# Performance work log

Hardware: AMD Instinct MI355X
Metric: run time of the kernel (lower is better)

## Reference

```python
import jax, jax.numpy as jnp
import numpy as np

EPS = 1e-5
DN = ('NCHW', 'OIHW', 'NCHW')

def _conv(x, w):
    return jax.lax.conv_general_dilated(x, w, (1, 1), 'SAME', dimension_numbers=DN)

def _bn(x, g, b, m, v):
    scale = (g * jax.lax.rsqrt(v + EPS)).reshape(1, -1, 1, 1)
    shift = (b - m * g * jax.lax.rsqrt(v + EPS)).reshape(1, -1, 1, 1)
    return x * scale + shift

def _convbn(x, w, g, b, m, v):
    return jax.nn.relu(_bn(_conv(x, w), g, b, m, v))

def _top_pool(x):
    # CornerNet TopPool: out[..., i, :] = max over rows >= i (reverse cummax along H)
    return jax.lax.cummax(x, axis=2, reverse=True)

def _left_pool(x):
    # CornerNet LeftPool: out[..., :, j] = max over cols >= j (reverse cummax along W)
    return jax.lax.cummax(x, axis=3, reverse=True)

def _mk_convbn(key, cin, cout, k):
    ks = jax.random.split(key, 5)
    w = jax.random.normal(ks[0], (cout, cin, k, k), jnp.float32) * (1.0 / np.sqrt(cin * k * k))
    g = jax.random.uniform(ks[1], (cout,), jnp.float32, 0.5, 1.5)
    b = jax.random.normal(ks[2], (cout,), jnp.float32) * 0.1
    m = jax.random.normal(ks[3], (cout,), jnp.float32) * 0.1
    v = jax.random.uniform(ks[4], (cout,), jnp.float32, 0.5, 1.5)
    return w, g, b, m, v

def setup_inputs() -> dict:
    key = jax.random.key(0)
    ks = jax.random.split(key, 12)
    dim, mid, B, H, W = 256, 128, 8, 128, 128
    d = {}
    d['x'] = jax.random.normal(ks[0], (B, dim, H, W), jnp.float32)
    for name, kk in [('lc1', ks[1]), ('p1c1', ks[2]), ('lc2', ks[3]), ('p2c1', ks[4])]:
        w, g, b, m, v = _mk_convbn(kk, dim, mid, 3)
        d[name + '_w'], d[name + '_g'], d[name + '_b'], d[name + '_m'], d[name + '_v'] = w, g, b, m, v
    d['p1lc_w'] = jax.random.normal(ks[5], (mid, mid, 3, 3), jnp.float32) * (1.0 / np.sqrt(mid * 9))
    d['p2lc_w'] = jax.random.normal(ks[6], (mid, mid, 3, 3), jnp.float32) * (1.0 / np.sqrt(mid * 9))
    w, g, b, m, v = _mk_convbn(ks[7], mid, dim, 3)
    d['pconv1_w'], d['pbn1_g'], d['pbn1_b'], d['pbn1_m'], d['pbn1_v'] = w, g, b, m, v
    w, g, b, m, v = _mk_convbn(ks[8], dim, dim, 1)
    d['conv1_w'], d['bn1_g'], d['bn1_b'], d['bn1_m'], d['bn1_v'] = w, g, b, m, v
    w, g, b, m, v = _mk_convbn(ks[9], dim, dim, 3)
    d['c2_w'], d['c2_g'], d['c2_b'], d['c2_m'], d['c2_v'] = w, g, b, m, v
    return d

def reference(x, lc1_w, lc1_g, lc1_b, lc1_m, lc1_v, p1c1_w, p1c1_g, p1c1_b, p1c1_m, p1c1_v, lc2_w, lc2_g, lc2_b, lc2_m, lc2_v, p2c1_w, p2c1_g, p2c1_b, p2c1_m, p2c1_v, p1lc_w, p2lc_w, pconv1_w, pbn1_g, pbn1_b, pbn1_m, pbn1_v, conv1_w, bn1_g, bn1_b, bn1_m, bn1_v, c2_w, c2_g, c2_b, c2_m, c2_v):
    look_conv1 = _convbn(x, lc1_w, lc1_g, lc1_b, lc1_m, lc1_v)
    p1_conv1 = _convbn(x, p1c1_w, p1c1_g, p1c1_b, p1c1_m, p1c1_v)
    look2 = _left_pool(look_conv1)
    p1_look = _conv(p1_conv1 + look2, p1lc_w)
    pool1 = _top_pool(p1_look)
    look_conv2 = _convbn(x, lc2_w, lc2_g, lc2_b, lc2_m, lc2_v)
    p2_conv1 = _convbn(x, p2c1_w, p2c1_g, p2c1_b, p2c1_m, p2c1_v)
    look1 = _top_pool(look_conv2)
    p2_look = _conv(p2_conv1 + look1, p2lc_w)
    pool2 = _left_pool(p2_look)
    p_bn1 = _bn(_conv(pool1 + pool2, pconv1_w), pbn1_g, pbn1_b, pbn1_m, pbn1_v)
    bn1 = _bn(_conv(x, conv1_w), bn1_g, bn1_b, bn1_m, bn1_v)
    relu1 = jax.nn.relu(p_bn1 + bn1)
    return _convbn(relu1, c2_w, c2_g, c2_b, c2_m, c2_v)
```

## Files before the change

### kernel.cpp

```cpp
#include <hip/hip_runtime.h>
#include <hip/hip_bf16.h>
#include <stdint.h>
#include <math.h>

typedef __bf16 bf16;
typedef __bf16 bf16x8 __attribute__((ext_vector_type(8)));
typedef float f32x4 __attribute__((ext_vector_type(4)));


__global__ void k_x_split(const float* __restrict__ in, bf16* __restrict__ out) {
  __shared__ float t[32][33];
  const int b = blockIdx.z;
  const int p0 = blockIdx.x << 5, c0 = blockIdx.y << 5;
  const int tx = threadIdx.x, ty = threadIdx.y;
  const float* ib = in + (size_t)b * 256 * 16384;
  bf16* ob = out + (size_t)b * 16384 * 512;
#pragma unroll
  for (int k = 0; k < 32; k += 8)
    t[ty + k][tx] = ib[(size_t)(c0 + ty + k) * 16384 + p0 + tx];
  __syncthreads();
#pragma unroll
  for (int k = 0; k < 32; k += 8) {
    float v = t[tx][ty + k];
    bf16 hv = (bf16)v;
    bf16 lv = (bf16)(v - (float)hv);
    ob[(size_t)(p0 + ty + k) * 512 + c0 + tx] = hv;
    ob[(size_t)(p0 + ty + k) * 512 + 256 + c0 + tx] = lv;
  }
}

__global__ void k_repack2(const float* __restrict__ src, bf16* __restrict__ dst,
                          int Cout, int Cin, int taps, int coutTotal, int coff) {
  int tid = blockIdx.x * 256 + threadIdx.x;
  int total = Cout * Cin * taps;
  if (tid >= total) return;
  int t = tid % taps;
  int rest = tid / taps;
  int ci = rest % Cin;
  int co = rest / Cin;
  float w = src[tid];
  bf16 wh = (bf16)w;
  bf16 wl = (bf16)(w - (float)wh);
  int nchunk = Cin >> 5;
  size_t segsz = (size_t)coutTotal * Cin;
  size_t base = (((size_t)(2 * t) * nchunk + (ci >> 5)) * coutTotal + coff + co) * 32
                + (ci & 31);
  dst[base] = wh;
  dst[base + segsz] = wl;
}

__global__ void k_bncoef(const float* __restrict__ g, const float* __restrict__ b,
                         const float* __restrict__ m, const float* __restrict__ v,
                         float* __restrict__ sc, float* __restrict__ sh, int n) {
  int c = blockIdx.x * 256 + threadIdx.x;
  if (c >= n) return;
  float s = g[c] * (1.0f / sqrtf(v[c] + 1e-5f));
  sc[c] = s;
  sh[c] = b[c] - m[c] * s;
}

template <int NTAPS>
__global__ __launch_bounds__(256, 3)
void k_conv(const bf16* __restrict__ in, int Cin, int rowStride,
            const bf16* __restrict__ Wr, int Cout,
            const float* __restrict__ scale, const float* __restrict__ shift,
            const bf16* __restrict__ addbuf, int relu,
            int out_mode, void* __restrict__ out) {
  constexpr int R = (NTAPS == 9) ? 3 : 1;
  __shared__ bf16 b_slab[2 * R * 132 * 32];
  const int bx = blockIdx.x;
  const int bb = bx & 7, h = (bx >> 3) & 127;
  const int row = bb * 128 + h;
  const int co_block = blockIdx.y << 7;
  const int tid = threadIdx.x;
  const int lane = tid & 63, wave = tid >> 6;
  const int wm = (wave >> 1) << 6, wn = (wave & 1) << 6;
  const int quad = lane >> 4, l15 = lane & 15;
  const int nchunk = Cin >> 5;
  const size_t segsz = (size_t)Cout * Cin;

  f32x4 acc[4][4];
#pragma unroll
  for (int i = 0; i < 4; ++i)
#pragma unroll
    for (int j = 0; j < 4; ++j)
#pragma unroll
      for (int r = 0; r < 4; ++r) acc[i][j][r] = 0.0f;

  {
    uint4 z; z.x = z.y = z.z = z.w = 0u;
    for (int u = tid; u < 2 * R * 2 * 4; u += 256) {
      int g = u & 3, e = (u >> 2) & 1, plane = u >> 3;
      bf16* d = &b_slab[((size_t)plane * 132 + (e ? 129 : 0)) * 32 + g * 8];
      *(uint4*)d = z;
    }
    if (R == 3 && (h == 0 || h == 127)) {
      int rr = (h == 0) ? 0 : 2;
      for (int u = tid; u < 2 * 132 * 4; u += 256) {
        int g = u & 3, p = (u >> 2) % 132, hl = (u >> 2) / 132;
        bf16* d = &b_slab[((size_t)(hl * R + rr) * 132 + p) * 32 + g * 8];
        *(uint4*)d = z;
      }
    }
  }

  for (int cb = 0; cb < Cin; cb += 32) {
    for (int u = wave; u < 2 * R * 8; u += 4) {
      int plane = u >> 3, sub = u & 7;
      int hl, rr;
      if (R == 3) { hl = plane >= 3; rr = plane - (hl ? 3 : 0); }
      else        { hl = plane; rr = 0; }
      int hi = h + rr - (R == 3 ? 1 : 0);
      if ((unsigned)hi < 128u) {
        int p = 1 + sub * 16 + (lane >> 2);
        int gsw = (lane & 3) ^ ((p >> 1) & 3);
        const bf16* src = in + (size_t)((bb * 128 + hi) * 128 + (p - 1)) * rowStride
                          + (size_t)hl * Cin + cb + gsw * 8;
        bf16* dst = &b_slab[(size_t)(plane * 132 + 1 + sub * 16) * 32];
        __builtin_amdgcn_global_load_lds(
            (const __attribute__((address_space(1))) uint32_t*)src,
            (__attribute__((address_space(3))) uint32_t*)dst, 16, 0, 0);
      }
    }
    __syncthreads();
#pragma unroll
    for (int tap = 0; tap < NTAPS; ++tap) {
      const int rr = (R == 3) ? (tap / 3) : 0;
      const int wc = (R == 3) ? (tap % 3) : 1;
      const int bH = rr * 132;
      const int bL = (R + rr) * 132;
      const int p0 = wn + l15 + wc;
      const int sw8 = (((p0 >> 1) & 3) ^ quad) << 3;
      const bf16* Ah = Wr + (((size_t)(2 * tap) * nchunk + (cb >> 5)) * Cout
                             + co_block + wm + l15) * 32 + quad * 8;
      const bf16* Al = Ah + segsz;
      bf16x8 afH[4], afL[4], bfH[4], bfL[4];
#pragma unroll
      for (int i = 0; i < 4; ++i) {
        afH[i] = *(const bf16x8*)(Ah + (size_t)i * 16 * 32);
        afL[i] = *(const bf16x8*)(Al + (size_t)i * 16 * 32);
      }
#pragma unroll
      for (int j = 0; j < 4; ++j) {
        const int p_idx = p0 + j * 16;
        bfH[j] = *(const bf16x8*)&b_slab[(size_t)(bH + p_idx) * 32 + sw8];
        bfL[j] = *(const bf16x8*)&b_slab[(size_t)(bL + p_idx) * 32 + sw8];
      }
#pragma unroll
      for (int i = 0; i < 4; ++i)
#pragma unroll
        for (int j = 0; j < 4; ++j) {
          acc[i][j] = __builtin_amdgcn_mfma_f32_16x16x32_bf16(afH[i], bfH[j], acc[i][j], 0, 0, 0);
          acc[i][j] = __builtin_amdgcn_mfma_f32_16x16x32_bf16(afH[i], bfL[j], acc[i][j], 0, 0, 0);
          acc[i][j] = __builtin_amdgcn_mfma_f32_16x16x32_bf16(afL[i], bfH[j], acc[i][j], 0, 0, 0);
        }
    }
    __syncthreads();
  }

#pragma unroll
  for (int i = 0; i < 4; ++i) {
    const int co = co_block + wm + i * 16 + (quad << 2);
#pragma unroll
    for (int j = 0; j < 4; ++j) {
      const int pos = wn + j * 16 + l15;
      float v[4];
#pragma unroll
      for (int r = 0; r < 4; ++r) v[r] = acc[i][j][r];
      if (scale) {
#pragma unroll
        for (int r = 0; r < 4; ++r) v[r] = v[r] * scale[co + r] + shift[co + r];
      }
      if (addbuf) {
        const bf16* ah = addbuf + (size_t)(row * 128 + pos) * (2 * Cout) + co;
        const bf16* al = ah + Cout;
#pragma unroll
        for (int r = 0; r < 4; ++r) v[r] += (float)ah[r] + (float)al[r];
      }
      if (relu) {
#pragma unroll
        for (int r = 0; r < 4; ++r) v[r] = fmaxf(v[r], 0.0f);
      }
      if (out_mode == 0) {
        bf16* ob = (bf16*)out;
        union { bf16 hv[4]; uint2 u; } ph, pl;
#pragma unroll
        for (int r = 0; r < 4; ++r) {
          ph.hv[r] = (bf16)v[r];
          pl.hv[r] = (bf16)(v[r] - (float)ph.hv[r]);
        }
        const size_t base = (size_t)(row * 128 + pos) * (2 * Cout);
        *(uint2*)&ob[base + co] = ph.u;
        *(uint2*)&ob[base + Cout + co] = pl.u;
      } else if (out_mode == 1) {
        float* of = (float*)out;
        float4 pk = make_float4(v[0], v[1], v[2], v[3]);
        *(float4*)&of[(size_t)(row * 128 + pos) * Cout + co] = pk;
      } else {
        float* of = (float*)out;
#pragma unroll
        for (int r = 0; r < 4; ++r)
          of[((size_t)(bb * Cout + co + r) * 128 + h) * 128 + pos] = v[r];
      }
    }
  }
}

__global__ void k_pool_s1(bf16* __restrict__ y) {
  int tid = blockIdx.x * 256 + threadIdx.x;
  int c = tid & 127, h = (tid >> 7) & 127, b = tid >> 14;
  bf16* base = y + (size_t)((b * 128 + h) * 128) * 512;
  float run = -INFINITY;
  for (int w = 127; w >= 0; --w) {
    bf16* p = base + (size_t)w * 512;
    float look = (float)p[c] + (float)p[256 + c];
    float padd = (float)p[128 + c] + (float)p[384 + c];
    run = fmaxf(run, look);
    float sum = run + padd;
    bf16 hv = (bf16)sum;
    p[c] = hv;
    p[128 + c] = (bf16)(sum - (float)hv);
  }
}
__global__ void k_pool_s2(bf16* __restrict__ y) {
  int tid = blockIdx.x * 256 + threadIdx.x;
  int c = tid & 127, w = (tid >> 7) & 127, b = tid >> 14;
  bf16* base = y + ((size_t)b * 16384 + w) * 512;
  float run = -INFINITY;
  for (int hh = 127; hh >= 0; --hh) {
    bf16* p = base + (size_t)hh * 65536;
    float look = (float)p[c] + (float)p[256 + c];
    float padd = (float)p[128 + c] + (float)p[384 + c];
    run = fmaxf(run, look);
    float sum = run + padd;
    bf16 hv = (bf16)sum;
    p[c] = hv;
    p[128 + c] = (bf16)(sum - (float)hv);
  }
}
__global__ void k_tpool_f(float* __restrict__ buf) {
  int tid = blockIdx.x * 256 + threadIdx.x;
  int c = tid & 127, w = (tid >> 7) & 127, b = tid >> 14;
  float* p = buf + ((size_t)b * 16384 + w) * 128 + c;
  float run = -INFINITY;
  for (int hh = 127; hh >= 0; --hh) {
    run = fmaxf(run, p[(size_t)hh * 16384]);
    p[(size_t)hh * 16384] = run;
  }
}
__global__ void k_lpool_add_f(const float* __restrict__ in, const float* __restrict__ addb,
                              bf16* __restrict__ out) {
  int tid = blockIdx.x * 256 + threadIdx.x;
  int c = tid & 127, h = (tid >> 7) & 127, b = tid >> 14;
  const float* p = in + (size_t)((b * 128 + h) * 128) * 128 + c;
  const float* a = addb + (size_t)((b * 128 + h) * 128) * 128 + c;
  bf16* o = out + (size_t)((b * 128 + h) * 128) * 256;
  float run = -INFINITY;
  for (int w = 127; w >= 0; --w) {
    run = fmaxf(run, p[(size_t)w * 128]);
    float sum = run + a[(size_t)w * 128];
    bf16 hv = (bf16)sum;
    o[(size_t)w * 256 + c] = hv;
    o[(size_t)w * 256 + 128 + c] = (bf16)(sum - (float)hv);
  }
}

extern "C" void kernel_launch(void* const* d_in, const int* in_sizes, int n_in,
                              void* d_out, int out_size, void* d_ws, size_t ws_size,
                              hipStream_t stream) {
  (void)in_sizes; (void)n_in; (void)out_size; (void)ws_size;
#define INF(i) ((const float*)d_in[i])
  char* ws = (char*)d_ws;
  const size_t MB = 1 << 20;
  bf16* wrA  = (bf16*)(ws + 0);
  bf16* wrB  = (bf16*)(ws + 2359296);
  bf16* wrp1 = (bf16*)(ws + 4718592);
  bf16* wrp2 = (bf16*)(ws + 5308416);
  bf16* wrpc = (bf16*)(ws + 5898240);
  bf16* wrc1 = (bf16*)(ws + 7077888);
  bf16* wrc2 = (bf16*)(ws + 7340032);
  float* scA  = (float*)(ws + 9699328);
  float* shA  = (float*)(ws + 9703424);
  float* scB  = (float*)(ws + 9707520);
  float* shB  = (float*)(ws + 9711616);
  float* scp  = (float*)(ws + 9715712);
  float* shp  = (float*)(ws + 9719808);
  float* scb  = (float*)(ws + 9723904);
  float* shb  = (float*)(ws + 9728000);
  float* scc2 = (float*)(ws + 9732096);
  float* shc2 = (float*)(ws + 9736192);
  bf16*  x_hl  = (bf16*)(ws + 10 * MB);
  bf16*  bnrel = (bf16*)(ws + 138 * MB);
  float* p1lk  = (float*)(ws + 266 * MB);
  float* p2lk  = (float*)(ws + 10 * MB);
  bf16*  psum  = (bf16*)(ws + 74 * MB);
  bf16*  yscr  = (bf16*)d_out;

  k_x_split<<<dim3(512, 8, 8), dim3(32, 8), 0, stream>>>(INF(0), x_hl);

  k_repack2<<<1152, 256, 0, stream>>>(INF(1),  wrA,  128, 256, 9, 256, 0);
  k_repack2<<<1152, 256, 0, stream>>>(INF(6),  wrA,  128, 256, 9, 256, 128);
  k_repack2<<<1152, 256, 0, stream>>>(INF(11), wrB,  128, 256, 9, 256, 0);
  k_repack2<<<1152, 256, 0, stream>>>(INF(16), wrB,  128, 256, 9, 256, 128);
  k_repack2<<<576,  256, 0, stream>>>(INF(21), wrp1, 128, 128, 9, 128, 0);
  k_repack2<<<576,  256, 0, stream>>>(INF(22), wrp2, 128, 128, 9, 128, 0);
  k_repack2<<<1152, 256, 0, stream>>>(INF(23), wrpc, 256, 128, 9, 256, 0);
  k_repack2<<<256,  256, 0, stream>>>(INF(28), wrc1, 256, 256, 1, 256, 0);
  k_repack2<<<2304, 256, 0, stream>>>(INF(33), wrc2, 256, 256, 9, 256, 0);

  k_bncoef<<<1, 256, 0, stream>>>(INF(2),  INF(3),  INF(4),  INF(5),  scA,       shA,       128);
  k_bncoef<<<1, 256, 0, stream>>>(INF(7),  INF(8),  INF(9),  INF(10), scA + 128, shA + 128, 128);
  k_bncoef<<<1, 256, 0, stream>>>(INF(12), INF(13), INF(14), INF(15), scB,       shB,       128);
  k_bncoef<<<1, 256, 0, stream>>>(INF(17), INF(18), INF(19), INF(20), scB + 128, shB + 128, 128);
  k_bncoef<<<1, 256, 0, stream>>>(INF(24), INF(25), INF(26), INF(27), scp, shp, 256);
  k_bncoef<<<1, 256, 0, stream>>>(INF(29), INF(30), INF(31), INF(32), scb, shb, 256);
  k_bncoef<<<1, 256, 0, stream>>>(INF(34), INF(35), INF(36), INF(37), scc2, shc2, 256);

  k_conv<1><<<dim3(1024, 2), 256, 0, stream>>>(x_hl, 256, 512, wrc1, 256, scb, shb, nullptr, 0, 0, bnrel);
  k_conv<9><<<dim3(1024, 2), 256, 0, stream>>>(x_hl, 256, 512, wrA, 256, scA, shA, nullptr, 1, 0, yscr);
  k_pool_s1<<<512, 256, 0, stream>>>(yscr);
  k_conv<9><<<dim3(1024, 1), 256, 0, stream>>>(yscr, 128, 512, wrp1, 128, nullptr, nullptr, nullptr, 0, 1, p1lk);
  k_conv<9><<<dim3(1024, 2), 256, 0, stream>>>(x_hl, 256, 512, wrB, 256, scB, shB, nullptr, 1, 0, yscr);
  k_pool_s2<<<512, 256, 0, stream>>>(yscr);
  k_conv<9><<<dim3(1024, 1), 256, 0, stream>>>(yscr, 128, 512, wrp2, 128, nullptr, nullptr, nullptr, 0, 1, p2lk);
  k_tpool_f<<<512, 256, 0, stream>>>(p1lk);
  k_lpool_add_f<<<512, 256, 0, stream>>>(p2lk, p1lk, psum);
  k_conv<9><<<dim3(1024, 2), 256, 0, stream>>>(psum, 128, 256, wrpc, 256, scp, shp, bnrel, 1, 0, bnrel);
  k_conv<9><<<dim3(1024, 2), 256, 0, stream>>>(bnrel, 256, 512, wrc2, 256, scc2, shc2, nullptr, 1, 2, (float*)d_out);
#undef INF
}
```

Measured before the change: 2.291 ms.

## Split staging into hi/lo halves and overlap next-chunk loads with MFMA

Restructures the conv main loop so the hi and lo halves of the bf16-split input are staged separately. The next chunk's hi half loads while the current lo-half MFMAs run, and vice versa, with manual vmcnt waits and raw s_barrier in place of full __syncthreads. Out-of-range rows are redirected to a dummy LDS buffer so every wave issues the same number of loads, which keeps the vmcnt counting uniform. It also raises wave priority around the MFMA blocks. The aim is to hide global-to-LDS latency behind compute, at the cost of fragile wait counts and a redundant extra load on the last iteration.

```diff
diff --git a/kernel.cpp b/kernel.cpp
--- a/kernel.cpp
+++ b/kernel.cpp
@@ -68,6 +68,7 @@
             int out_mode, void* __restrict__ out) {
   constexpr int R = (NTAPS == 9) ? 3 : 1;
   __shared__ bf16 b_slab[2 * R * 132 * 32];
+  __shared__ bf16 dummy_lds[512];
   const int bx = blockIdx.x;
   const int bb = bx & 7, h = (bx >> 3) & 127;
   const int row = bb * 128 + h;
@@ -103,60 +104,105 @@
       }
     }
   }
+  __syncthreads();
+
+  auto stage_half = [&](int hl, int cb) {
+    for (int u = wave; u < R * 8; u += 4) {
+      int rr = u >> 3, sub = u & 7;
+      int plane = hl * R + rr;
+      int hi = h + rr - (R == 3 ? 1 : 0);
+      bool ok = (unsigned)hi < 128u;
+      int hic = ok ? hi : h;
+      int p = 1 + sub * 16 + (lane >> 2);
+      int gsw = (lane & 3) ^ ((p >> 1) & 3);
+      const bf16* src = in + (size_t)((bb * 128 + hic) * 128 + (p - 1)) * rowStride
+                        + (size_t)hl * Cin + cb + gsw * 8;
+      bf16* dst = ok ? &b_slab[(size_t)(plane * 132 + 1 + sub * 16) * 32]
+                     : dummy_lds;
+      __builtin_amdgcn_global_load_lds(
+          (const __attribute__((address_space(1))) uint32_t*)src,
+          (__attribute__((address_space(3))) uint32_t*)dst, 16, 0, 0);
+    }
+  };
+
+#define WAIT_VM()                                                        \
+  do {                                                                   \
+    __builtin_amdgcn_sched_barrier(0);                                   \
+    if constexpr (R == 3) asm volatile("s_waitcnt vmcnt(6)" ::: "memory"); \
+    else                  asm volatile("s_waitcnt vmcnt(2)" ::: "memory"); \
+    __builtin_amdgcn_sched_barrier(0);                                   \
+  } while (0)
+
+  stage_half(0, 0);
+  stage_half(1, 0);
 
   for (int cb = 0; cb < Cin; cb += 32) {
-    for (int u = wave; u < 2 * R * 8; u += 4) {
-      int plane = u >> 3, sub = u & 7;
-      int hl, rr;
-      if (R == 3) { hl = plane >= 3; rr = plane - (hl ? 3 : 0); }
-      else        { hl = plane; rr = 0; }
-      int hi = h + rr - (R == 3 ? 1 : 0);
-      if ((unsigned)hi < 128u) {
-        int p = 1 + sub * 16 + (lane >> 2);
-        int gsw = (lane & 3) ^ ((p >> 1) & 3);
-        const bf16* src = in + (size_t)((bb * 128 + hi) * 128 + (p - 1)) * rowStride
-                          + (size_t)hl * Cin + cb + gsw * 8;
-        bf16* dst = &b_slab[(size_t)(plane * 132 + 1 + sub * 16) * 32];
-        __builtin_amdgcn_global_load_lds(
-            (const __attribute__((address_space(1))) uint32_t*)src,
-            (__attribute__((address_space(3))) uint32_t*)dst, 16, 0, 0);
-      }
-    }
-    __syncthreads();
+    WAIT_VM();
+    __builtin_amdgcn_s_barrier();
 #pragma unroll
     for (int tap = 0; tap < NTAPS; ++tap) {
       const int rr = (R == 3) ? (tap / 3) : 0;
       const int wc = (R == 3) ? (tap % 3) : 1;
       const int bH = rr * 132;
+      const int p0 = wn + l15 + wc;
+      const int sw8 = (((p0 >> 1) & 3) ^ quad) << 3;
+      const bf16* Ah = Wr + (((size_t)(2 * tap) * nchunk + (cb >> 5)) * Cout
+                             + co_block + wm + l15) * 32 + quad * 8;
+      const bf16* Al = Ah + segsz;
+      bf16x8 afH[4], afL[4], bfH[4];
+#pragma unroll
+      for (int i = 0; i < 4; ++i) {
+        afH[i] = *(const bf16x8*)(Ah + (size_t)i * 16 * 32);
+        afL[i] = *(const bf16x8*)(Al + (size_t)i * 16 * 32);
+      }
+#pragma unroll
+      for (int j = 0; j < 4; ++j)
+        bfH[j] = *(const bf16x8*)&b_slab[(size_t)(bH + p0 + j * 16) * 32 + sw8];
+      __builtin_amdgcn_s_setprio(1);
+#pragma unroll
+      for (int i = 0; i < 4; ++i)
+#pragma unroll
+        for (int j = 0; j < 4; ++j) {
+          acc[i][j] = __builtin_amdgcn_mfma_f32_16x16x32_bf16(afH[i], bfH[j], acc[i][j], 0, 0, 0);
+          acc[i][j] = __builtin_amdgcn_mfma_f32_16x16x32_bf16(afL[i], bfH[j], acc[i][j], 0, 0, 0);
+        }
+      __builtin_amdgcn_s_setprio(0);
+    }
+    __builtin_amdgcn_s_barrier();
+    {
+      int nb = (cb + 32 < Cin) ? cb + 32 : cb;
+      stage_half(0, nb);
+    }
+    WAIT_VM();
+    __builtin_amdgcn_s_barrier();
+#pragma unroll
+    for (int tap = 0; tap < NTAPS; ++tap) {
+      const int rr = (R == 3) ? (tap / 3) : 0;
+      const int wc = (R == 3) ? (tap % 3) : 1;
       const int bL = (R + rr) * 132;
       const int p0 = wn + l15 + wc;
       const int sw8 = (((p0 >> 1) & 3) ^ quad) << 3;
       const bf16* Ah = Wr + (((size_t)(2 * tap) * nchunk + (cb >> 5)) * Cout
                              + co_block + wm + l15) * 32 + quad * 8;
-      const bf16* Al = Ah + segsz;
-      bf16x8 afH[4], afL[4], bfH[4], bfL[4];
-#pragma unroll
-      for (int i = 0; i < 4; ++i) {
+      bf16x8 afH[4], bfL[4];
+#pragma unroll
+      for (int i = 0; i < 4; ++i)
         afH[i] = *(const bf16x8*)(Ah + (size_t)i * 16 * 32);
-        afL[i] = *(const bf16x8*)(Al + (size_t)i * 16 * 32);
-      }
-#pragma unroll
-      for (int j = 0; j < 4; ++j) {
-        const int p_idx = p0 + j * 16;
-        bfH[j] = *(const bf16x8*)&b_slab[(size_t)(bH + p_idx) * 32 + sw8];
-        bfL[j] = *(const bf16x8*)&b_slab[(size_t)(bL + p_idx) * 32 + sw8];
-      }
+#pragma unroll
+      for (int j = 0; j < 4; ++j)
+        bfL[j] = *(const bf16x8*)&b_slab[(size_t)(bL + p0 + j * 16) * 32 + sw8];
+      __builtin_amdgcn_s_setprio(1);
 #pragma unroll
       for (int i = 0; i < 4; ++i)
 #pragma unroll
-        for (int j = 0; j < 4; ++j) {
-          acc[i][j] = __builtin_amdgcn_mfma_f32_16x16x32_bf16(afH[i], bfH[j], acc[i][j], 0, 0, 0);
+        for (int j = 0; j < 4; ++j)
           acc[i][j] = __builtin_amdgcn_mfma_f32_16x16x32_bf16(afH[i], bfL[j], acc[i][j], 0, 0, 0);
-          acc[i][j] = __builtin_amdgcn_mfma_f32_16x16x32_bf16(afL[i], bfH[j], acc[i][j], 0, 0, 0);
-        }
-    }
-    __syncthreads();
-  }
+      __builtin_amdgcn_s_setprio(0);
+    }
+    __builtin_amdgcn_s_barrier();
+    if (cb + 32 < Cin) stage_half(1, cb + 32);
+  }
+#undef WAIT_VM
 
 #pragma unroll
   for (int i = 0; i < 4; ++i) {
```

Result: slower. 2.598 ms (+13.4%).

## Split conv tiles to half-width rows and double-buffer LDS input staging

Applied to the files above, without the earlier changes.

The conv kernel now covers 64 output pixels per block instead of a full 128-pixel row, so twice as many blocks launch. Each wave owns 32 output channels across all 64 pixels. The input slab is double-buffered in LDS and the next channel chunk's global_load_lds is issued during the last tap's MFMAs, so loads overlap compute and one barrier per chunk is dropped. In exchange, the halo column is loaded separately and per-block tiles are smaller, which raises weight reloads and lowers MFMA reuse per B fragment.

```diff
diff --git a/kernel.cpp b/kernel.cpp
--- a/kernel.cpp
+++ b/kernel.cpp
@@ -67,21 +67,23 @@
             const bf16* __restrict__ addbuf, int relu,
             int out_mode, void* __restrict__ out) {
   constexpr int R = (NTAPS == 9) ? 3 : 1;
-  __shared__ bf16 b_slab[2 * R * 132 * 32];
+  constexpr int PL = 2 * R;
+  constexpr int BUF = PL * 66 * 32;
+  __shared__ bf16 b_slab[2 * BUF];
   const int bx = blockIdx.x;
   const int bb = bx & 7, h = (bx >> 3) & 127;
+  const int w0 = (bx >> 10) << 6;
   const int row = bb * 128 + h;
   const int co_block = blockIdx.y << 7;
   const int tid = threadIdx.x;
   const int lane = tid & 63, wave = tid >> 6;
-  const int wm = (wave >> 1) << 6, wn = (wave & 1) << 6;
   const int quad = lane >> 4, l15 = lane & 15;
   const int nchunk = Cin >> 5;
   const size_t segsz = (size_t)Cout * Cin;
 
-  f32x4 acc[4][4];
-#pragma unroll
-  for (int i = 0; i < 4; ++i)
+  f32x4 acc[2][4];
+#pragma unroll
+  for (int i = 0; i < 2; ++i)
 #pragma unroll
     for (int j = 0; j < 4; ++j)
 #pragma unroll
@@ -89,65 +91,91 @@
 
   {
     uint4 z; z.x = z.y = z.z = z.w = 0u;
-    for (int u = tid; u < 2 * R * 2 * 4; u += 256) {
-      int g = u & 3, e = (u >> 2) & 1, plane = u >> 3;
-      bf16* d = &b_slab[((size_t)plane * 132 + (e ? 129 : 0)) * 32 + g * 8];
+    for (int u = tid; u < 2 * PL * 2 * 4; u += 256) {
+      int g = u & 3, e = (u >> 2) & 1, plane = (u >> 3) % PL, bs = u / (PL * 8);
+      bf16* d = &b_slab[(size_t)bs * BUF + ((size_t)plane * 66 + (e ? 65 : 0)) * 32 + g * 8];
       *(uint4*)d = z;
     }
     if (R == 3 && (h == 0 || h == 127)) {
       int rr = (h == 0) ? 0 : 2;
-      for (int u = tid; u < 2 * 132 * 4; u += 256) {
-        int g = u & 3, p = (u >> 2) % 132, hl = (u >> 2) / 132;
-        bf16* d = &b_slab[((size_t)(hl * R + rr) * 132 + p) * 32 + g * 8];
+      for (int u = tid; u < 2 * 2 * 66 * 4; u += 256) {
+        int g = u & 3, p = (u >> 2) % 66, hl = ((u >> 2) / 66) & 1, bs = u / (2 * 66 * 4);
+        bf16* d = &b_slab[(size_t)bs * BUF + ((size_t)(hl * R + rr) * 66 + p) * 32 + g * 8];
         *(uint4*)d = z;
       }
     }
   }
 
-  for (int cb = 0; cb < Cin; cb += 32) {
-    for (int u = wave; u < 2 * R * 8; u += 4) {
-      int plane = u >> 3, sub = u & 7;
-      int hl, rr;
-      if (R == 3) { hl = plane >= 3; rr = plane - (hl ? 3 : 0); }
-      else        { hl = plane; rr = 0; }
+  const int s0 = (w0 == 0) ? 1 : 0;
+  const int pt = (w0 == 0) ? 65 : 64;
+  const int wt = w0 + pt - 1;
+
+  auto stage = [&](bf16* buf, int cb) {
+    for (int u = wave; u < PL * 4; u += 4) {
+      int plane = u >> 2, sub = u & 3;
+      int hl = plane >= R ? 1 : 0, rr = plane - hl * R;
       int hi = h + rr - (R == 3 ? 1 : 0);
       if ((unsigned)hi < 128u) {
-        int p = 1 + sub * 16 + (lane >> 2);
+        int p = s0 + sub * 16 + (lane >> 2);
         int gsw = (lane & 3) ^ ((p >> 1) & 3);
-        const bf16* src = in + (size_t)((bb * 128 + hi) * 128 + (p - 1)) * rowStride
+        const bf16* src = in + (size_t)((bb * 128 + hi) * 128 + (w0 + p - 1)) * rowStride
                           + (size_t)hl * Cin + cb + gsw * 8;
-        bf16* dst = &b_slab[(size_t)(plane * 132 + 1 + sub * 16) * 32];
+        bf16* dst = buf + ((size_t)plane * 66 + s0 + sub * 16) * 32;
         __builtin_amdgcn_global_load_lds(
             (const __attribute__((address_space(1))) uint32_t*)src,
             (__attribute__((address_space(3))) uint32_t*)dst, 16, 0, 0);
       }
     }
-    __syncthreads();
+    if (lane < 4) {
+      for (int plane = wave; plane < PL; plane += 4) {
+        int hl = plane >= R ? 1 : 0, rr = plane - hl * R;
+        int hi = h + rr - (R == 3 ? 1 : 0);
+        if ((unsigned)hi < 128u) {
+          int gsw = lane ^ ((pt >> 1) & 3);
+          const bf16* src = in + (size_t)((bb * 128 + hi) * 128 + wt) * rowStride
+                            + (size_t)hl * Cin + cb + gsw * 8;
+          bf16* dst = buf + ((size_t)plane * 66 + pt) * 32;
+          __builtin_amdgcn_global_load_lds(
+              (const __attribute__((address_space(1))) uint32_t*)src,
+              (__attribute__((address_space(3))) uint32_t*)dst, 16, 0, 0);
+        }
+      }
+    }
+  };
+
+  stage(b_slab, 0);
+  __syncthreads();
+
+  int cur = 0;
+  for (int cb = 0; cb < Cin; cb += 32) {
+    bf16* bufc = b_slab + (size_t)cur * BUF;
 #pragma unroll
     for (int tap = 0; tap < NTAPS; ++tap) {
       const int rr = (R == 3) ? (tap / 3) : 0;
       const int wc = (R == 3) ? (tap % 3) : 1;
-      const int bH = rr * 132;
-      const int bL = (R + rr) * 132;
-      const int p0 = wn + l15 + wc;
+      const int p0 = l15 + wc;
       const int sw8 = (((p0 >> 1) & 3) ^ quad) << 3;
-      const bf16* Ah = Wr + (((size_t)(2 * tap) * nchunk + (cb >> 5)) * Cout
-                             + co_block + wm + l15) * 32 + quad * 8;
-      const bf16* Al = Ah + segsz;
-      bf16x8 afH[4], afL[4], bfH[4], bfL[4];
-#pragma unroll
-      for (int i = 0; i < 4; ++i) {
-        afH[i] = *(const bf16x8*)(Ah + (size_t)i * 16 * 32);
-        afL[i] = *(const bf16x8*)(Al + (size_t)i * 16 * 32);
+      const bf16* Af = Wr + (((size_t)(2 * tap) * nchunk + (cb >> 5)) * Cout
+                             + co_block + wave * 32 + l15) * 32 + quad * 8;
+      bf16x8 afH[2], afL[2], bfH[4], bfL[4];
+#pragma unroll
+      for (int i = 0; i < 2; ++i) {
+        afH[i] = *(const bf16x8*)(Af + (size_t)i * 16 * 32);
+        afL[i] = *(const bf16x8*)(Af + segsz + (size_t)i * 16 * 32);
       }
 #pragma unroll
       for (int j = 0; j < 4; ++j) {
         const int p_idx = p0 + j * 16;
-        bfH[j] = *(const bf16x8*)&b_slab[(size_t)(bH + p_idx) * 32 + sw8];
-        bfL[j] = *(const bf16x8*)&b_slab[(size_t)(bL + p_idx) * 32 + sw8];
-      }
-#pragma unroll
-      for (int i = 0; i < 4; ++i)
+        bfH[j] = *(const bf16x8*)&bufc[((size_t)rr * 66 + p_idx) * 32 + sw8];
+        bfL[j] = *(const bf16x8*)&bufc[((size_t)(R + rr) * 66 + p_idx) * 32 + sw8];
+      }
+      if (tap == NTAPS - 1 && cb + 32 < Cin) {
+        __builtin_amdgcn_sched_barrier(0);
+        stage(b_slab + (size_t)(cur ^ 1) * BUF, cb + 32);
+        __builtin_amdgcn_sched_barrier(0);
+      }
+#pragma unroll
+      for (int i = 0; i < 2; ++i)
 #pragma unroll
         for (int j = 0; j < 4; ++j) {
           acc[i][j] = __builtin_amdgcn_mfma_f32_16x16x32_bf16(afH[i], bfH[j], acc[i][j], 0, 0, 0);
@@ -156,14 +184,15 @@
         }
     }
     __syncthreads();
-  }
-
-#pragma unroll
-  for (int i = 0; i < 4; ++i) {
-    const int co = co_block + wm + i * 16 + (quad << 2);
+    cur ^= 1;
+  }
+
+#pragma unroll
+  for (int i = 0; i < 2; ++i) {
+    const int co = co_block + wave * 32 + i * 16 + (quad << 2);
 #pragma unroll
     for (int j = 0; j < 4; ++j) {
-      const int pos = wn + j * 16 + l15;
+      const int pos = w0 + j * 16 + l15;
       float v[4];
 #pragma unroll
       for (int r = 0; r < 4; ++r) v[r] = acc[i][j][r];
@@ -316,16 +345,16 @@
   k_bncoef<<<1, 256, 0, stream>>>(INF(29), INF(30), INF(31), INF(32), scb, shb, 256);
   k_bncoef<<<1, 256, 0, stream>>>(INF(34), INF(35), INF(36), INF(37), scc2, shc2, 256);
 
-  k_conv<1><<<dim3(1024, 2), 256, 0, stream>>>(x_hl, 256, 512, wrc1, 256, scb, shb, nullptr, 0, 0, bnrel);
-  k_conv<9><<<dim3(1024, 2), 256, 0, stream>>>(x_hl, 256, 512, wrA, 256, scA, shA, nullptr, 1, 0, yscr);
+  k_conv<1><<<dim3(2048, 2), 256, 0, stream>>>(x_hl, 256, 512, wrc1, 256, scb, shb, nullptr, 0, 0, bnrel);
+  k_conv<9><<<dim3(2048, 2), 256, 0, stream>>>(x_hl, 256, 512, wrA, 256, scA, shA, nullptr, 1, 0, yscr);
   k_pool_s1<<<512, 256, 0, stream>>>(yscr);
-  k_conv<9><<<dim3(1024, 1), 256, 0, stream>>>(yscr, 128, 512, wrp1, 128, nullptr, nullptr, nullptr, 0, 1, p1lk);
-  k_conv<9><<<dim3(1024, 2), 256, 0, stream>>>(x_hl, 256, 512, wrB, 256, scB, shB, nullptr, 1, 0, yscr);
+  k_conv<9><<<dim3(2048, 1), 256, 0, stream>>>(yscr, 128, 512, wrp1, 128, nullptr, nullptr, nullptr, 0, 1, p1lk);
+  k_conv<9><<<dim3(2048, 2), 256, 0, stream>>>(x_hl, 256, 512, wrB, 256, scB, shB, nullptr, 1, 0, yscr);
   k_pool_s2<<<512, 256, 0, stream>>>(yscr);
-  k_conv<9><<<dim3(1024, 1), 256, 0, stream>>>(yscr, 128, 512, wrp2, 128, nullptr, nullptr, nullptr, 0, 1, p2lk);
+  k_conv<9><<<dim3(2048, 1), 256, 0, stream>>>(yscr, 128, 512, wrp2, 128, nullptr, nullptr, nullptr, 0, 1, p2lk);
   k_tpool_f<<<512, 256, 0, stream>>>(p1lk);
   k_lpool_add_f<<<512, 256, 0, stream>>>(p2lk, p1lk, psum);
-  k_conv<9><<<dim3(1024, 2), 256, 0, stream>>>(psum, 128, 256, wrpc, 256, scp, shp, bnrel, 1, 0, bnrel);
-  k_conv<9><<<dim3(1024, 2), 256, 0, stream>>>(bnrel, 256, 512, wrc2, 256, scc2, shc2, nullptr, 1, 2, (float*)d_out);
+  k_conv<9><<<dim3(2048, 2), 256, 0, stream>>>(psum, 128, 256, wrpc, 256, scp, shp, bnrel, 1, 0, bnrel);
+  k_conv<9><<<dim3(2048, 2), 256, 0, stream>>>(bnrel, 256, 512, wrc2, 256, scc2, shc2, nullptr, 1, 2, (float*)d_out);
 #undef INF
 }
```

After: 2.206 ms. 1.04x faster.
